# Optimization experiments

Hardware: AMD Instinct MI355X
Metric: run time of the kernel (lower is better)

Reference implementation:

```python
import jax, jax.numpy as jnp
import numpy as np

BETA = 0.25  # commitment/codebook mixing as in VQVAE.__init__


def setup_inputs() -> dict:
    key = jax.random.key(0)
    k1, k2 = jax.random.split(key)
    # z: encoder latent [B, C, H, W] with C = latent_dim
    z = jax.random.normal(k1, (32, 64, 64, 64), dtype=jnp.float32)
    # codebook: nn.Embedding(num_embeddings, latent_dim).weight
    codebook = jax.random.normal(k2, (1024, 64), dtype=jnp.float32)
    return {"z": z, "codebook": codebook}


def reference(z, codebook):
    B, C, H, W = z.shape
    zf = z.reshape(B, C, H * W).transpose(0, 2, 1)  # [B, N, C], N = H*W
    # Squared Euclidean distances; argmin identical to torch.cdist(p=2) argmin
    # since sqrt is monotone (min_distances are unused in the original forward).
    d2 = (jnp.sum(zf * zf, axis=-1, keepdims=True)              # [B, N, 1]
          + jnp.sum(codebook * codebook, axis=-1)[None, None, :]  # [1, 1, K]
          - 2.0 * jnp.einsum('bnc,kc->bnk', zf, codebook))        # [B, N, K]
    indices = jnp.argmin(d2, axis=-1)                            # [B, N]
    z_q = codebook[indices]                                      # [B, N, C] gather
    z_q = z_q.transpose(0, 2, 1).reshape(B, C, H, W)
    commitment_loss = jnp.mean((jax.lax.stop_gradient(z_q) - z) ** 2)
    codebook_loss = jnp.mean((z_q - jax.lax.stop_gradient(z)) ** 2)
    loss = commitment_loss + BETA * codebook_loss
    return z_q, loss
```

## Files before the change

kernel.cpp:

```cpp
#include <hip/hip_runtime.h>
#include <float.h>

#define HW    4096
#define NC    64
#define NK    1024
#define NB    32
#define NPIX  (NB*HW)
#define TOTAL (NPIX*NC)
#define PPB   128

#define MARGIN 8e-3f

typedef __attribute__((ext_vector_type(8))) short short8;
typedef __attribute__((ext_vector_type(4))) float floatx4;

__device__ __forceinline__ unsigned short f2bf(float f) {
    unsigned u = __float_as_uint(f);
    u += 0x7FFFu + ((u >> 16) & 1u);
    return (unsigned short)(u >> 16);
}
__device__ __forceinline__ float bf2f(unsigned short h) {
    return __uint_as_float(((unsigned)h) << 16);
}

__global__ void vq_prep_kernel(const float* __restrict__ cb,
                               float* __restrict__ cnorm,
                               unsigned short* __restrict__ cb_hi,
                               unsigned short* __restrict__ cb_lo,
                               float* __restrict__ loss_out) {
    const int b = blockIdx.x;
    if (b < 64) {
        const int i = b * 256 + threadIdx.x;
        if (i == 0) loss_out[0] = 0.0f;
        float4 v = ((const float4*)cb)[i];
        unsigned short h0 = f2bf(v.x), h1 = f2bf(v.y),
                       h2 = f2bf(v.z), h3 = f2bf(v.w);
        unsigned short l0 = f2bf(v.x - bf2f(h0)), l1 = f2bf(v.y - bf2f(h1)),
                       l2 = f2bf(v.z - bf2f(h2)), l3 = f2bf(v.w - bf2f(h3));
        uint2 ph = make_uint2((unsigned)h0 | ((unsigned)h1 << 16),
                              (unsigned)h2 | ((unsigned)h3 << 16));
        uint2 pl = make_uint2((unsigned)l0 | ((unsigned)l1 << 16),
                              (unsigned)l2 | ((unsigned)l3 << 16));
        ((uint2*)cb_hi)[i] = ph;
        ((uint2*)cb_lo)[i] = pl;
    } else {
        const int k = (b - 64) * 256 + threadIdx.x;
        const float4* r4 = (const float4*)(cb + (size_t)k * NC);
        double s = 0.0;
        #pragma unroll
        for (int j = 0; j < 16; ++j) {
            float4 v = r4[j];
            s = fma((double)v.x, (double)v.x, s);
            s = fma((double)v.y, (double)v.y, s);
            s = fma((double)v.z, (double)v.z, s);
            s = fma((double)v.w, (double)v.w, s);
        }
        cnorm[k] = (float)s;
    }
}

__global__ __launch_bounds__(512, 8) void vq_mfma_kernel(
        const float* __restrict__ z,
        const float* __restrict__ cb,
        const unsigned short* __restrict__ cb_hi,
        const unsigned short* __restrict__ cb_lo,
        const float* __restrict__ cnorm,
        float* __restrict__ zq,
        float* __restrict__ loss_out) {
    __shared__ alignas(16) uint4  abuf[2][1024];
    __shared__ alignas(16) float  cn_lds[NK];
    __shared__ int   finidx[PPB];
    __shared__ int   flags[PPB];
    __shared__ float redf[8];

    const int tid = threadIdx.x;
    const int g0  = blockIdx.x * PPB;
    const int bb  = g0 >> 12;
    const int pp0 = g0 & 4095;
    const float* zbase = z  + (size_t)bb * (NC * HW) + pp0;
    float*      zqbase = zq + (size_t)bb * (NC * HW) + pp0;

    ((float2*)cn_lds)[tid] = ((const float2*)cnorm)[tid];

    const int lane = tid & 63;
    const int w    = tid >> 6;
    const int q    = lane >> 4;
    const int pcol = lane & 15;

    auto src_of = [&](int s) -> const char* {
        const int tt = s >> 8, part = (s >> 7) & 1;
        const int row = (s >> 3) & 15, chunk = s & 7;
        const char* bp = part ? (const char*)cb_lo : (const char*)cb_hi;
        return bp + tt * 2048 + row * 128 + ((chunk ^ (row & 7)) * 16);
    };
    const char* gsrc1 = src_of(tid);
    const char* gsrc2 = src_of(tid + 512);

    auto stage_iv = [&](int iv, int buf) {
        __builtin_amdgcn_global_load_lds(
            (const __attribute__((address_space(1))) void*)
                (gsrc1 + (size_t)iv * 8192),
            (__attribute__((address_space(3))) void*)&abuf[buf][tid],
            16, 0, 0);
        __builtin_amdgcn_global_load_lds(
            (const __attribute__((address_space(1))) void*)
                (gsrc2 + (size_t)iv * 8192),
            (__attribute__((address_space(3))) void*)&abuf[buf][tid + 512],
            16, 0, 0);
    };

    stage_iv(0, 0);

    float zraw[2][8];
    #pragma unroll
    for (int ks = 0; ks < 2; ++ks)
        #pragma unroll
        for (int t = 0; t < 8; ++t)
            zraw[ks][t] = zbase[(size_t)(ks * 32 + q * 8 + t) * HW
                                + (w * 16 + pcol)];
    short8 Bh[2], Bl[2];
    #pragma unroll
    for (int ks = 0; ks < 2; ++ks)
        #pragma unroll
        for (int t = 0; t < 8; ++t) {
            float v = -2.0f * zraw[ks][t];
            unsigned short h = f2bf(v);
            unsigned short l = f2bf(v - bf2f(h));
            Bh[ks][t] = (short)h;
            Bl[ks][t] = (short)l;
        }

    const int ridx0 = pcol * 8 + (q ^ (pcol & 7));
    const int ridx1 = pcol * 8 + ((4 + q) ^ (pcol & 7));

    __syncthreads();

    float B1 = FLT_MAX, B2 = FLT_MAX;
    int   I1 = 0;

    for (int iv = 0; iv < 16; ++iv) {
        if (iv < 15) stage_iv(iv + 1, (iv + 1) & 1);
        const short8* Abase = (const short8*)&abuf[iv & 1][0];
        #pragma unroll
        for (int tt = 0; tt < 4; ++tt) {
            const short8* A = Abase + tt * 256;
            short8 ah0 = A[ridx0];
            short8 ah1 = A[ridx1];
            short8 al0 = A[128 + ridx0];
            short8 al1 = A[128 + ridx1];
            const int tile = iv * 4 + tt;
            const floatx4 cn4 = *(const floatx4*)&cn_lds[tile * 16 + q * 4];
            const int kb = tile * 16 + q * 4;
            floatx4 a0 = __builtin_amdgcn_mfma_f32_16x16x32_bf16(ah0, Bh[0], cn4, 0, 0, 0);
            floatx4 a1 = {0.f, 0.f, 0.f, 0.f};
            a1 = __builtin_amdgcn_mfma_f32_16x16x32_bf16(ah1, Bh[1], a1, 0, 0, 0);
            a0 = __builtin_amdgcn_mfma_f32_16x16x32_bf16(ah0, Bl[0], a0, 0, 0, 0);
            a1 = __builtin_amdgcn_mfma_f32_16x16x32_bf16(ah1, Bl[1], a1, 0, 0, 0);
            a0 = __builtin_amdgcn_mfma_f32_16x16x32_bf16(al0, Bh[0], a0, 0, 0, 0);
            a1 = __builtin_amdgcn_mfma_f32_16x16x32_bf16(al1, Bh[1], a1, 0, 0, 0);

            #pragma unroll
            for (int i = 0; i < 4; ++i) {
                float s = a0[i] + a1[i];
                bool lt = s < B1;
                I1 = lt ? (kb + i) : I1;
                B2 = __builtin_amdgcn_fmed3f(s, B1, B2);
                B1 = fminf(s, B1);
            }
        }
        __syncthreads();
    }

    {
        float b1 = B1, b2 = B2;
        int i1 = I1;
        #pragma unroll
        for (int d = 16; d <= 32; d <<= 1) {
            float ob1 = __shfl_xor(b1, d);
            float ob2 = __shfl_xor(b2, d);
            int   oi1 = __shfl_xor(i1, d);
            float nb2 = fminf(fmaxf(b1, ob1), fminf(b2, ob2));
            bool lt = (ob1 < b1) || (ob1 == b1 && oi1 < i1);
            b1 = lt ? ob1 : b1;
            i1 = lt ? oi1 : i1;
            b2 = nb2;
        }
        if (q == 0) {
            const int px = w * 16 + pcol;
            finidx[px] = i1;
            flags[px]  = (b2 - b1 < MARGIN) ? 1 : 0;
        }
    }
    int myflag = 0;
    __syncthreads();
    if (tid < PPB) myflag = flags[tid];
    const int nflag = __syncthreads_count(myflag);

    if (nflag > 0) {
        double* red_s = reinterpret_cast<double*>(cn_lds);
        int*    red_i = reinterpret_cast<int*>(&abuf[0][0]);
        for (int p = 0; p < PPB; ++p) {
            if (flags[p]) {
                const float* zp = zbase + p;
                double bd = 1.0e300; int bi = 0;
                #pragma unroll 1
                for (int r = 0; r < 2; ++r) {
                    const int k = tid * 2 + r;
                    const float* rowp = cb + (size_t)k * NC;
                    double s = 0.0;
                    for (int c = 0; c < NC; ++c) {
                        double t = (double)zp[(size_t)c * HW] - (double)rowp[c];
                        s = fma(t, t, s);
                    }
                    if (s < bd) { bd = s; bi = k; }
                }
                red_s[tid] = bd; red_i[tid] = bi;
                __syncthreads();
                if (tid < 64) {
                    double m = red_s[tid]; int mi = red_i[tid];
                    #pragma unroll
                    for (int t = 1; t < 8; ++t) {
                        double om = red_s[tid + 64 * t];
                        int    oi = red_i[tid + 64 * t];
                        if (om < m || (om == m && oi < mi)) { m = om; mi = oi; }
                    }
                    #pragma unroll
                    for (int off = 32; off > 0; off >>= 1) {
                        double om = __shfl_down(m, off);
                        int    oi = __shfl_down(mi, off);
                        if (om < m || (om == m && oi < mi)) { m = om; mi = oi; }
                    }
                    if (tid == 0) finidx[p] = mi;
                }
                __syncthreads();
            }
        }
        __syncthreads();
    }

    {
        const int p  = tid & (PPB - 1);
        const int qq = tid >> 7;
        const int fi = finidx[p];
        const float4* crow4 = (const float4*)(cb + (size_t)fi * NC) + qq * 4;
        float sse = 0.f;
        #pragma unroll
        for (int j = 0; j < 4; ++j) {
            const float4 qv = crow4[j];
            const size_t c0 = (size_t)(qq * 16 + 4 * j) * HW + p;
            const float z0 = zbase[c0];
            const float z1 = zbase[c0 + HW];
            const float z2 = zbase[c0 + 2 * (size_t)HW];
            const float z3 = zbase[c0 + 3 * (size_t)HW];
            zqbase[c0]                  = qv.x;
            zqbase[c0 + HW]             = qv.y;
            zqbase[c0 + 2 * (size_t)HW] = qv.z;
            zqbase[c0 + 3 * (size_t)HW] = qv.w;
            float t0 = qv.x - z0, t1 = qv.y - z1, t2 = qv.z - z2, t3 = qv.w - z3;
            sse = fmaf(t0, t0, sse);
            sse = fmaf(t1, t1, sse);
            sse = fmaf(t2, t2, sse);
            sse = fmaf(t3, t3, sse);
        }
        #pragma unroll
        for (int off = 32; off > 0; off >>= 1) sse += __shfl_down(sse, off);
        if ((tid & 63) == 0) redf[tid >> 6] = sse;
        __syncthreads();
        if (tid == 0) {
            float tot = 0.f;
            #pragma unroll
            for (int r = 0; r < 8; ++r) tot += redf[r];
            atomicAdd(loss_out, tot * (1.25f / (float)TOTAL));
        }
    }
}

extern "C" void kernel_launch(void* const* d_in, const int* in_sizes, int n_in,
                              void* d_out, int out_size, void* d_ws, size_t ws_size,
                              hipStream_t stream) {
    const float* z  = (const float*)d_in[0];
    const float* cb = (const float*)d_in[1];
    float* out      = (float*)d_out;
    float* zqp      = out;
    float* loss     = out + TOTAL;

    float* cnorm          = (float*)d_ws;
    unsigned short* cb_hi = (unsigned short*)((char*)d_ws + 4096);
    unsigned short* cb_lo = (unsigned short*)((char*)d_ws + 4096 + NK * NC * 2);

    vq_prep_kernel<<<68, 256, 0, stream>>>(cb, cnorm, cb_hi, cb_lo, loss);
    vq_mfma_kernel<<<NPIX / PPB, 512, 0, stream>>>(z, cb, cb_hi, cb_lo, cnorm,
                                                   zqp, loss);
}
```

Baseline: 174.9 us.

## Switch distance MFMA to fp16 with split-z only and adaptive error margin

Replaces the three-product bf16 hi/lo split (codebook hi+lo, z hi+lo) with fp16 MFMA, using a single fp16 codebook copy and a hi/lo split only on z. This halves the codebook LDS staging and cuts MFMAs per tile from six to four. To keep the argmin exact, the prep kernel computes the maximum codebook fp16 rounding error and the main kernel derives a per-pixel margin from it and the pixel's norm. Pixels inside that margin fall back to the exact recheck. The risk is that a looser margin flags more pixels for the slow exact path.

```diff
diff --git a/kernel.cpp b/kernel.cpp
--- a/kernel.cpp
+++ b/kernel.cpp
@@ -9,44 +9,38 @@
 #define TOTAL (NPIX*NC)
 #define PPB   128
 
-#define MARGIN 8e-3f
-
-typedef __attribute__((ext_vector_type(8))) short short8;
-typedef __attribute__((ext_vector_type(4))) float floatx4;
-
-__device__ __forceinline__ unsigned short f2bf(float f) {
-    unsigned u = __float_as_uint(f);
-    u += 0x7FFFu + ((u >> 16) & 1u);
-    return (unsigned short)(u >> 16);
-}
-__device__ __forceinline__ float bf2f(unsigned short h) {
-    return __uint_as_float(((unsigned)h) << 16);
+#define SLACK 0.03f
+
+typedef __attribute__((ext_vector_type(8))) _Float16 f16x8;
+typedef __attribute__((ext_vector_type(4))) float   floatx4;
+
+__device__ __forceinline__ unsigned short f2h_bits(float f) {
+    _Float16 h = (_Float16)f;
+    union { _Float16 h; unsigned short u; } c; c.h = h;
+    return c.u;
 }
 
 __global__ void vq_prep_kernel(const float* __restrict__ cb,
                                float* __restrict__ cnorm,
-                               unsigned short* __restrict__ cb_hi,
-                               unsigned short* __restrict__ cb_lo,
+                               unsigned short* __restrict__ cb_h,
+                               float* __restrict__ e2max,
                                float* __restrict__ loss_out) {
     const int b = blockIdx.x;
     if (b < 64) {
         const int i = b * 256 + threadIdx.x;
         if (i == 0) loss_out[0] = 0.0f;
         float4 v = ((const float4*)cb)[i];
-        unsigned short h0 = f2bf(v.x), h1 = f2bf(v.y),
-                       h2 = f2bf(v.z), h3 = f2bf(v.w);
-        unsigned short l0 = f2bf(v.x - bf2f(h0)), l1 = f2bf(v.y - bf2f(h1)),
-                       l2 = f2bf(v.z - bf2f(h2)), l3 = f2bf(v.w - bf2f(h3));
+        unsigned short h0 = f2h_bits(v.x), h1 = f2h_bits(v.y),
+                       h2 = f2h_bits(v.z), h3 = f2h_bits(v.w);
         uint2 ph = make_uint2((unsigned)h0 | ((unsigned)h1 << 16),
                               (unsigned)h2 | ((unsigned)h3 << 16));
-        uint2 pl = make_uint2((unsigned)l0 | ((unsigned)l1 << 16),
-                              (unsigned)l2 | ((unsigned)l3 << 16));
-        ((uint2*)cb_hi)[i] = ph;
-        ((uint2*)cb_lo)[i] = pl;
+        ((uint2*)cb_h)[i] = ph;
     } else {
+        __shared__ float wmax[4];
         const int k = (b - 64) * 256 + threadIdx.x;
         const float4* r4 = (const float4*)(cb + (size_t)k * NC);
         double s = 0.0;
+        float  e2 = 0.0f;
         #pragma unroll
         for (int j = 0; j < 16; ++j) {
             float4 v = r4[j];
@@ -54,20 +48,34 @@
             s = fma((double)v.y, (double)v.y, s);
             s = fma((double)v.z, (double)v.z, s);
             s = fma((double)v.w, (double)v.w, s);
+            float l0 = v.x - (float)(_Float16)v.x;
+            float l1 = v.y - (float)(_Float16)v.y;
+            float l2 = v.z - (float)(_Float16)v.z;
+            float l3 = v.w - (float)(_Float16)v.w;
+            e2 = fmaf(l0, l0, e2); e2 = fmaf(l1, l1, e2);
+            e2 = fmaf(l2, l2, e2); e2 = fmaf(l3, l3, e2);
         }
         cnorm[k] = (float)s;
+        #pragma unroll
+        for (int off = 32; off > 0; off >>= 1)
+            e2 = fmaxf(e2, __shfl_down(e2, off));
+        if ((threadIdx.x & 63) == 0) wmax[threadIdx.x >> 6] = e2;
+        __syncthreads();
+        if (threadIdx.x == 0)
+            e2max[b - 64] = fmaxf(fmaxf(wmax[0], wmax[1]),
+                                  fmaxf(wmax[2], wmax[3]));
     }
 }
 
 __global__ __launch_bounds__(512, 8) void vq_mfma_kernel(
         const float* __restrict__ z,
         const float* __restrict__ cb,
-        const unsigned short* __restrict__ cb_hi,
-        const unsigned short* __restrict__ cb_lo,
+        const unsigned short* __restrict__ cb_h,
         const float* __restrict__ cnorm,
+        const float* __restrict__ e2max,
         float* __restrict__ zq,
         float* __restrict__ loss_out) {
-    __shared__ alignas(16) uint4  abuf[2][1024];
+    __shared__ alignas(16) uint4  abuf[2][512];
     __shared__ alignas(16) float  cn_lds[NK];
     __shared__ int   finidx[PPB];
     __shared__ int   flags[PPB];
@@ -87,25 +95,19 @@
     const int q    = lane >> 4;
     const int pcol = lane & 15;
 
-    auto src_of = [&](int s) -> const char* {
-        const int tt = s >> 8, part = (s >> 7) & 1;
-        const int row = (s >> 3) & 15, chunk = s & 7;
-        const char* bp = part ? (const char*)cb_lo : (const char*)cb_hi;
-        return bp + tt * 2048 + row * 128 + ((chunk ^ (row & 7)) * 16);
-    };
-    const char* gsrc1 = src_of(tid);
-    const char* gsrc2 = src_of(tid + 512);
+    {
+    }
+    const int  stt   = tid >> 7;
+    const int  srow  = (tid >> 3) & 15;
+    const int  schk  = tid & 7;
+    const char* gsrc = (const char*)cb_h + stt * 2048 + srow * 128
+                       + ((schk ^ (srow & 7)) * 16);
 
     auto stage_iv = [&](int iv, int buf) {
         __builtin_amdgcn_global_load_lds(
             (const __attribute__((address_space(1))) void*)
-                (gsrc1 + (size_t)iv * 8192),
+                (gsrc + (size_t)iv * 8192),
             (__attribute__((address_space(3))) void*)&abuf[buf][tid],
-            16, 0, 0);
-        __builtin_amdgcn_global_load_lds(
-            (const __attribute__((address_space(1))) void*)
-                (gsrc2 + (size_t)iv * 8192),
-            (__attribute__((address_space(3))) void*)&abuf[buf][tid + 512],
             16, 0, 0);
     };
 
@@ -118,17 +120,31 @@
         for (int t = 0; t < 8; ++t)
             zraw[ks][t] = zbase[(size_t)(ks * 32 + q * 8 + t) * HW
                                 + (w * 16 + pcol)];
-    short8 Bh[2], Bl[2];
+
+    float nz2 = 0.0f;
     #pragma unroll
     for (int ks = 0; ks < 2; ++ks)
         #pragma unroll
+        for (int t = 0; t < 8; ++t)
+            nz2 = fmaf(zraw[ks][t], zraw[ks][t], nz2);
+    nz2 += __shfl_xor(nz2, 16);
+    nz2 += __shfl_xor(nz2, 32);
+
+    f16x8 Bh[2], Bl[2];
+    #pragma unroll
+    for (int ks = 0; ks < 2; ++ks)
+        #pragma unroll
         for (int t = 0; t < 8; ++t) {
             float v = -2.0f * zraw[ks][t];
-            unsigned short h = f2bf(v);
-            unsigned short l = f2bf(v - bf2f(h));
-            Bh[ks][t] = (short)h;
-            Bl[ks][t] = (short)l;
-        }
+            _Float16 vh = (_Float16)v;
+            _Float16 vl = (_Float16)(v - (float)vh);
+            Bh[ks][t] = vh;
+            Bl[ks][t] = vl;
+        }
+
+    const float e2m = fmaxf(fmaxf(e2max[0], e2max[1]),
+                            fmaxf(e2max[2], e2max[3]));
+    const float margin = 4.0f * sqrtf(e2m) * sqrtf(nz2) + SLACK;
 
     const int ridx0 = pcol * 8 + (q ^ (pcol & 7));
     const int ridx1 = pcol * 8 + ((4 + q) ^ (pcol & 7));
@@ -140,28 +156,22 @@
 
     for (int iv = 0; iv < 16; ++iv) {
         if (iv < 15) stage_iv(iv + 1, (iv + 1) & 1);
-        const short8* Abase = (const short8*)&abuf[iv & 1][0];
         #pragma unroll
         for (int tt = 0; tt < 4; ++tt) {
-            const short8* A = Abase + tt * 256;
-            short8 ah0 = A[ridx0];
-            short8 ah1 = A[ridx1];
-            short8 al0 = A[128 + ridx0];
-            short8 al1 = A[128 + ridx1];
+            const f16x8* A = (const f16x8*)&abuf[iv & 1][tt * 128];
+            f16x8 ah0 = A[ridx0];
+            f16x8 ah1 = A[ridx1];
             const int tile = iv * 4 + tt;
             const floatx4 cn4 = *(const floatx4*)&cn_lds[tile * 16 + q * 4];
             const int kb = tile * 16 + q * 4;
-            floatx4 a0 = __builtin_amdgcn_mfma_f32_16x16x32_bf16(ah0, Bh[0], cn4, 0, 0, 0);
-            floatx4 a1 = {0.f, 0.f, 0.f, 0.f};
-            a1 = __builtin_amdgcn_mfma_f32_16x16x32_bf16(ah1, Bh[1], a1, 0, 0, 0);
-            a0 = __builtin_amdgcn_mfma_f32_16x16x32_bf16(ah0, Bl[0], a0, 0, 0, 0);
-            a1 = __builtin_amdgcn_mfma_f32_16x16x32_bf16(ah1, Bl[1], a1, 0, 0, 0);
-            a0 = __builtin_amdgcn_mfma_f32_16x16x32_bf16(al0, Bh[0], a0, 0, 0, 0);
-            a1 = __builtin_amdgcn_mfma_f32_16x16x32_bf16(al1, Bh[1], a1, 0, 0, 0);
+            floatx4 a = __builtin_amdgcn_mfma_f32_16x16x32_f16(ah0, Bh[0], cn4, 0, 0, 0);
+            a = __builtin_amdgcn_mfma_f32_16x16x32_f16(ah0, Bl[0], a, 0, 0, 0);
+            a = __builtin_amdgcn_mfma_f32_16x16x32_f16(ah1, Bh[1], a, 0, 0, 0);
+            a = __builtin_amdgcn_mfma_f32_16x16x32_f16(ah1, Bl[1], a, 0, 0, 0);
 
             #pragma unroll
             for (int i = 0; i < 4; ++i) {
-                float s = a0[i] + a1[i];
+                float s = a[i];
                 bool lt = s < B1;
                 I1 = lt ? (kb + i) : I1;
                 B2 = __builtin_amdgcn_fmed3f(s, B1, B2);
@@ -188,7 +198,7 @@
         if (q == 0) {
             const int px = w * 16 + pcol;
             finidx[px] = i1;
-            flags[px]  = (b2 - b1 < MARGIN) ? 1 : 0;
+            flags[px]  = (b2 - b1 < margin) ? 1 : 0;
         }
     }
     int myflag = 0;
@@ -285,10 +295,10 @@
     float* loss     = out + TOTAL;
 
     float* cnorm          = (float*)d_ws;
-    unsigned short* cb_hi = (unsigned short*)((char*)d_ws + 4096);
-    unsigned short* cb_lo = (unsigned short*)((char*)d_ws + 4096 + NK * NC * 2);
-
-    vq_prep_kernel<<<68, 256, 0, stream>>>(cb, cnorm, cb_hi, cb_lo, loss);
-    vq_mfma_kernel<<<NPIX / PPB, 512, 0, stream>>>(z, cb, cb_hi, cb_lo, cnorm,
+    float* e2max          = (float*)((char*)d_ws + 4096);
+    unsigned short* cb_h  = (unsigned short*)((char*)d_ws + 8192);
+
+    vq_prep_kernel<<<68, 256, 0, stream>>>(cb, cnorm, cb_h, e2max, loss);
+    vq_mfma_kernel<<<NPIX / PPB, 512, 0, stream>>>(z, cb, cb_h, cnorm, e2max,
                                                    zqp, loss);
 }
```

New measurement: 299.0 us. +71.0%, slower.

## Fuse codebook prep into main VQ kernel, converting bf16 hi/lo on the fly

Applied to the files above, without the earlier changes.

Removes the separate prep kernel. Each block now computes codebook norms into LDS itself and converts fp32 codebook tiles to bf16 hi/lo pairs while staging them into LDS. Loss zeroing moves to a hipMemsetAsync. This saves one launch and the workspace round-trip. The cost is redundant per-block work: 1024 blocks each recompute all 1024 norms and the conversions, and staging goes through registers instead of the async global_load_lds. The norm also drops from double to float precision, which could change near-tie argmin results.

```diff
diff --git a/kernel.cpp b/kernel.cpp
--- a/kernel.cpp
+++ b/kernel.cpp
@@ -23,48 +23,9 @@
     return __uint_as_float(((unsigned)h) << 16);
 }
 
-__global__ void vq_prep_kernel(const float* __restrict__ cb,
-                               float* __restrict__ cnorm,
-                               unsigned short* __restrict__ cb_hi,
-                               unsigned short* __restrict__ cb_lo,
-                               float* __restrict__ loss_out) {
-    const int b = blockIdx.x;
-    if (b < 64) {
-        const int i = b * 256 + threadIdx.x;
-        if (i == 0) loss_out[0] = 0.0f;
-        float4 v = ((const float4*)cb)[i];
-        unsigned short h0 = f2bf(v.x), h1 = f2bf(v.y),
-                       h2 = f2bf(v.z), h3 = f2bf(v.w);
-        unsigned short l0 = f2bf(v.x - bf2f(h0)), l1 = f2bf(v.y - bf2f(h1)),
-                       l2 = f2bf(v.z - bf2f(h2)), l3 = f2bf(v.w - bf2f(h3));
-        uint2 ph = make_uint2((unsigned)h0 | ((unsigned)h1 << 16),
-                              (unsigned)h2 | ((unsigned)h3 << 16));
-        uint2 pl = make_uint2((unsigned)l0 | ((unsigned)l1 << 16),
-                              (unsigned)l2 | ((unsigned)l3 << 16));
-        ((uint2*)cb_hi)[i] = ph;
-        ((uint2*)cb_lo)[i] = pl;
-    } else {
-        const int k = (b - 64) * 256 + threadIdx.x;
-        const float4* r4 = (const float4*)(cb + (size_t)k * NC);
-        double s = 0.0;
-        #pragma unroll
-        for (int j = 0; j < 16; ++j) {
-            float4 v = r4[j];
-            s = fma((double)v.x, (double)v.x, s);
-            s = fma((double)v.y, (double)v.y, s);
-            s = fma((double)v.z, (double)v.z, s);
-            s = fma((double)v.w, (double)v.w, s);
-        }
-        cnorm[k] = (float)s;
-    }
-}
-
 __global__ __launch_bounds__(512, 8) void vq_mfma_kernel(
         const float* __restrict__ z,
         const float* __restrict__ cb,
-        const unsigned short* __restrict__ cb_hi,
-        const unsigned short* __restrict__ cb_lo,
-        const float* __restrict__ cnorm,
         float* __restrict__ zq,
         float* __restrict__ loss_out) {
     __shared__ alignas(16) uint4  abuf[2][1024];
@@ -80,33 +41,56 @@
     const float* zbase = z  + (size_t)bb * (NC * HW) + pp0;
     float*      zqbase = zq + (size_t)bb * (NC * HW) + pp0;
 
-    ((float2*)cn_lds)[tid] = ((const float2*)cnorm)[tid];
-
     const int lane = tid & 63;
     const int w    = tid >> 6;
     const int q    = lane >> 4;
     const int pcol = lane & 15;
 
-    auto src_of = [&](int s) -> const char* {
-        const int tt = s >> 8, part = (s >> 7) & 1;
-        const int row = (s >> 3) & 15, chunk = s & 7;
-        const char* bp = part ? (const char*)cb_lo : (const char*)cb_hi;
-        return bp + tt * 2048 + row * 128 + ((chunk ^ (row & 7)) * 16);
-    };
-    const char* gsrc1 = src_of(tid);
-    const char* gsrc2 = src_of(tid + 512);
+    #pragma unroll
+    for (int r = 0; r < 2; ++r) {
+        const int k = tid * 2 + r;
+        const float4* r4 = (const float4*)(cb + (size_t)k * NC);
+        float4 acc = {0.f, 0.f, 0.f, 0.f};
+        #pragma unroll
+        for (int j = 0; j < 16; ++j) {
+            float4 v = r4[j];
+            acc.x = fmaf(v.x, v.x, acc.x);
+            acc.y = fmaf(v.y, v.y, acc.y);
+            acc.z = fmaf(v.z, v.z, acc.z);
+            acc.w = fmaf(v.w, v.w, acc.w);
+        }
+        cn_lds[k] = (acc.x + acc.y) + (acc.z + acc.w);
+    }
+
+    const int stt  = tid >> 7;
+    const int srow = (tid >> 3) & 15;
+    const int schk = tid & 7;
+    const float4* gsrc4 = (const float4*)(cb + ((size_t)stt * 16 + srow) * NC
+                                          + schk * 8);
+    const int wslot = stt * 256 + srow * 8 + (schk ^ (srow & 7));
 
     auto stage_iv = [&](int iv, int buf) {
-        __builtin_amdgcn_global_load_lds(
-            (const __attribute__((address_space(1))) void*)
-                (gsrc1 + (size_t)iv * 8192),
-            (__attribute__((address_space(3))) void*)&abuf[buf][tid],
-            16, 0, 0);
-        __builtin_amdgcn_global_load_lds(
-            (const __attribute__((address_space(1))) void*)
-                (gsrc2 + (size_t)iv * 8192),
-            (__attribute__((address_space(3))) void*)&abuf[buf][tid + 512],
-            16, 0, 0);
+        const float4 v0 = gsrc4[(size_t)iv * 1024];
+        const float4 v1 = gsrc4[(size_t)iv * 1024 + 1];
+        unsigned short h0 = f2bf(v0.x), h1 = f2bf(v0.y),
+                       h2 = f2bf(v0.z), h3 = f2bf(v0.w),
+                       h4 = f2bf(v1.x), h5 = f2bf(v1.y),
+                       h6 = f2bf(v1.z), h7 = f2bf(v1.w);
+        unsigned short l0 = f2bf(v0.x - bf2f(h0)), l1 = f2bf(v0.y - bf2f(h1)),
+                       l2 = f2bf(v0.z - bf2f(h2)), l3 = f2bf(v0.w - bf2f(h3)),
+                       l4 = f2bf(v1.x - bf2f(h4)), l5 = f2bf(v1.y - bf2f(h5)),
+                       l6 = f2bf(v1.z - bf2f(h6)), l7 = f2bf(v1.w - bf2f(h7));
+        uint4 ph, pl;
+        ph.x = (unsigned)h0 | ((unsigned)h1 << 16);
+        ph.y = (unsigned)h2 | ((unsigned)h3 << 16);
+        ph.z = (unsigned)h4 | ((unsigned)h5 << 16);
+        ph.w = (unsigned)h6 | ((unsigned)h7 << 16);
+        pl.x = (unsigned)l0 | ((unsigned)l1 << 16);
+        pl.y = (unsigned)l2 | ((unsigned)l3 << 16);
+        pl.z = (unsigned)l4 | ((unsigned)l5 << 16);
+        pl.w = (unsigned)l6 | ((unsigned)l7 << 16);
+        abuf[buf][wslot]       = ph;
+        abuf[buf][wslot + 128] = pl;
     };
 
     stage_iv(0, 0);
@@ -140,10 +124,9 @@
 
     for (int iv = 0; iv < 16; ++iv) {
         if (iv < 15) stage_iv(iv + 1, (iv + 1) & 1);
-        const short8* Abase = (const short8*)&abuf[iv & 1][0];
         #pragma unroll
         for (int tt = 0; tt < 4; ++tt) {
-            const short8* A = Abase + tt * 256;
+            const short8* A = (const short8*)&abuf[iv & 1][tt * 256];
             short8 ah0 = A[ridx0];
             short8 ah1 = A[ridx1];
             short8 al0 = A[128 + ridx0];
@@ -284,11 +267,6 @@
     float* zqp      = out;
     float* loss     = out + TOTAL;
 
-    float* cnorm          = (float*)d_ws;
-    unsigned short* cb_hi = (unsigned short*)((char*)d_ws + 4096);
-    unsigned short* cb_lo = (unsigned short*)((char*)d_ws + 4096 + NK * NC * 2);
-
-    vq_prep_kernel<<<68, 256, 0, stream>>>(cb, cnorm, cb_hi, cb_lo, loss);
-    vq_mfma_kernel<<<NPIX / PPB, 512, 0, stream>>>(z, cb, cb_hi, cb_lo, cnorm,
-                                                   zqp, loss);
-}
+    hipMemsetAsync(loss, 0, sizeof(float), stream);
+    vq_mfma_kernel<<<NPIX / PPB, 512, 0, stream>>>(z, cb, zqp, loss);
+}
```

New measurement: 208.5 us. 1.19x slower.
